# Performance work log

Hardware: AMD Instinct MI355X
Metric: run time of the kernel (lower is better)

Reference implementation:

```python
import jax, jax.numpy as jnp
import numpy as np

B = 2_000_000   # batch of affine transforms
N = 3           # spatial ndims -> flattened transform has N*(N+1)=12 entries


def setup_inputs() -> dict:
    key = jax.random.key(0)
    # small shifts so that identity + shift is always invertible
    trf = jax.random.normal(key, (B, N * (N + 1)), dtype=jnp.float32) * 0.1
    return {"trf": trf}


def reference(trf):
    """Batched equivalent of tf.map_fn(_single_invert, trf).

    Per sample: lift flattened (N,N+1) shift to an (N+1,N+1) matrix over the
    identity, invert it, and convert back to a flattened shift.
    """
    b = trf.shape[0]
    eye = jnp.eye(N + 1, dtype=trf.dtype)
    # affine_shift_to_identity: (b, N, N+1) -> pad zero row -> add identity
    mat = trf.reshape(b, N, N + 1)
    full = jnp.concatenate(
        [mat, jnp.zeros((b, 1, N + 1), dtype=trf.dtype)], axis=1
    ) + eye                                  # (b, N+1, N+1)
    inv = jnp.linalg.inv(full)               # batched tiny inversions
    # affine_identity_to_shift: subtract identity, drop last row, flatten
    shift = (inv - eye)[:, :N, :]            # (b, N, N+1)
    return shift.reshape(b, N * (N + 1))
```

## Files before the change

kernel.cpp:

```cpp
#include <hip/hip_runtime.h>


typedef float nfloat4 __attribute__((ext_vector_type(4)));

__global__ __launch_bounds__(256, 8) void invert_affine_kernel(
    const float4* __restrict__ in, float4* __restrict__ out, int b) {
  __shared__ float4 buf[768];

  const int tid = threadIdx.x;
  const int base_s = blockIdx.x * 256;
  const int base_f4 = base_s * 3;
  const int n_f4 = b * 3;

#pragma unroll
  for (int k = 0; k < 3; ++k) {
    int idx = base_f4 + k * 256 + tid;
    if (idx < n_f4) {
      nfloat4 nv = __builtin_nontemporal_load((const nfloat4*)&in[idx]);
      buf[k * 256 + tid] = make_float4(nv.x, nv.y, nv.z, nv.w);
    }
  }
  __syncthreads();

  const int s = base_s + tid;
  if (s < b) {
    float4 r0 = buf[tid * 3 + 0];
    float4 r1 = buf[tid * 3 + 1];
    float4 r2 = buf[tid * 3 + 2];

    float a00 = r0.x + 1.0f, a01 = r0.y,        a02 = r0.z,        t0 = r0.w;
    float a10 = r1.x,        a11 = r1.y + 1.0f, a12 = r1.z,        t1 = r1.w;
    float a20 = r2.x,        a21 = r2.y,        a22 = r2.z + 1.0f, t2 = r2.w;

    float b00 = a11 * a22 - a12 * a21;
    float b01 = a02 * a21 - a01 * a22;
    float b02 = a01 * a12 - a02 * a11;
    float b10 = a12 * a20 - a10 * a22;
    float b11 = a00 * a22 - a02 * a20;
    float b12 = a02 * a10 - a00 * a12;
    float b20 = a10 * a21 - a11 * a20;
    float b21 = a01 * a20 - a00 * a21;
    float b22 = a00 * a11 - a01 * a10;

    float det = a00 * b00 + a01 * b10 + a02 * b20;
    float rdet = 1.0f / det;

    b00 *= rdet; b01 *= rdet; b02 *= rdet;
    b10 *= rdet; b11 *= rdet; b12 *= rdet;
    b20 *= rdet; b21 *= rdet; b22 *= rdet;

    buf[tid * 3 + 0] = make_float4(b00 - 1.0f, b01, b02,
                                   -(b00 * t0 + b01 * t1 + b02 * t2));
    buf[tid * 3 + 1] = make_float4(b10, b11 - 1.0f, b12,
                                   -(b10 * t0 + b11 * t1 + b12 * t2));
    buf[tid * 3 + 2] = make_float4(b20, b21, b22 - 1.0f,
                                   -(b20 * t0 + b21 * t1 + b22 * t2));
  }
  __syncthreads();

#pragma unroll
  for (int k = 0; k < 3; ++k) {
    int idx = base_f4 + k * 256 + tid;
    if (idx < n_f4) {
      float4 vv = buf[k * 256 + tid];
      nfloat4 nv;
      nv.x = vv.x; nv.y = vv.y; nv.z = vv.z; nv.w = vv.w;
      __builtin_nontemporal_store(nv, (nfloat4*)&out[idx]);
    }
  }
}

extern "C" void kernel_launch(void* const* d_in, const int* in_sizes, int n_in,
                              void* d_out, int out_size, void* d_ws, size_t ws_size,
                              hipStream_t stream) {
  const float4* trf = (const float4*)d_in[0];
  float4* out = (float4*)d_out;
  int b = in_sizes[0] / 12;
  const int threads = 256;
  int blocks = (b + threads - 1) / threads;
  invert_affine_kernel<<<blocks, threads, 0, stream>>>(trf, out, b);
}
```

Before: 160.3 us.

## Use per-wave shared buffers with wave barriers and two samples per thread

Each block is split into four independent waves, and each wave stages 128 samples in its own slice of shared memory. This lets the block-wide __syncthreads be replaced by wave-level barriers. Every thread now processes two samples, so half as many blocks are launched, and the occupancy hint drops from 8 to 6. The aim is to remove block-level synchronisation stalls and per-block overhead in this memory-bound kernel. The cost is more shared memory per block, which may lower occupancy.

```diff
diff --git a/kernel.cpp b/kernel.cpp
--- a/kernel.cpp
+++ b/kernel.cpp
@@ -3,66 +3,73 @@
 
 typedef float nfloat4 __attribute__((ext_vector_type(4)));
 
-__global__ __launch_bounds__(256, 8) void invert_affine_kernel(
+__global__ __launch_bounds__(256, 6) void invert_affine_kernel(
     const float4* __restrict__ in, float4* __restrict__ out, int b) {
-  __shared__ float4 buf[768];
+  __shared__ float4 buf[4][384];
 
-  const int tid = threadIdx.x;
-  const int base_s = blockIdx.x * 256;
-  const int base_f4 = base_s * 3;
+  const int wave = threadIdx.x >> 6;
+  const int lane = threadIdx.x & 63;
+  float4* wbuf = buf[wave];
+
+  const int s0 = blockIdx.x * 512 + wave * 128;
+  const int base_f4 = s0 * 3;
   const int n_f4 = b * 3;
 
 #pragma unroll
-  for (int k = 0; k < 3; ++k) {
-    int idx = base_f4 + k * 256 + tid;
+  for (int k = 0; k < 6; ++k) {
+    const int idx = base_f4 + k * 64 + lane;
     if (idx < n_f4) {
       nfloat4 nv = __builtin_nontemporal_load((const nfloat4*)&in[idx]);
-      buf[k * 256 + tid] = make_float4(nv.x, nv.y, nv.z, nv.w);
+      wbuf[k * 64 + lane] = make_float4(nv.x, nv.y, nv.z, nv.w);
     }
   }
-  __syncthreads();
-
-  const int s = base_s + tid;
-  if (s < b) {
-    float4 r0 = buf[tid * 3 + 0];
-    float4 r1 = buf[tid * 3 + 1];
-    float4 r2 = buf[tid * 3 + 2];
-
-    float a00 = r0.x + 1.0f, a01 = r0.y,        a02 = r0.z,        t0 = r0.w;
-    float a10 = r1.x,        a11 = r1.y + 1.0f, a12 = r1.z,        t1 = r1.w;
-    float a20 = r2.x,        a21 = r2.y,        a22 = r2.z + 1.0f, t2 = r2.w;
-
-    float b00 = a11 * a22 - a12 * a21;
-    float b01 = a02 * a21 - a01 * a22;
-    float b02 = a01 * a12 - a02 * a11;
-    float b10 = a12 * a20 - a10 * a22;
-    float b11 = a00 * a22 - a02 * a20;
-    float b12 = a02 * a10 - a00 * a12;
-    float b20 = a10 * a21 - a11 * a20;
-    float b21 = a01 * a20 - a00 * a21;
-    float b22 = a00 * a11 - a01 * a10;
-
-    float det = a00 * b00 + a01 * b10 + a02 * b20;
-    float rdet = 1.0f / det;
-
-    b00 *= rdet; b01 *= rdet; b02 *= rdet;
-    b10 *= rdet; b11 *= rdet; b12 *= rdet;
-    b20 *= rdet; b21 *= rdet; b22 *= rdet;
-
-    buf[tid * 3 + 0] = make_float4(b00 - 1.0f, b01, b02,
-                                   -(b00 * t0 + b01 * t1 + b02 * t2));
-    buf[tid * 3 + 1] = make_float4(b10, b11 - 1.0f, b12,
-                                   -(b10 * t0 + b11 * t1 + b12 * t2));
-    buf[tid * 3 + 2] = make_float4(b20, b21, b22 - 1.0f,
-                                   -(b20 * t0 + b21 * t1 + b22 * t2));
-  }
-  __syncthreads();
+  __builtin_amdgcn_wave_barrier();
 
 #pragma unroll
-  for (int k = 0; k < 3; ++k) {
-    int idx = base_f4 + k * 256 + tid;
+  for (int si = 0; si < 2; ++si) {
+    const int s = s0 + si * 64 + lane;
+    if (s < b) {
+      const int o = (si * 64 + lane) * 3;
+      float4 r0 = wbuf[o + 0];
+      float4 r1 = wbuf[o + 1];
+      float4 r2 = wbuf[o + 2];
+
+      float a00 = r0.x + 1.0f, a01 = r0.y,        a02 = r0.z,        t0 = r0.w;
+      float a10 = r1.x,        a11 = r1.y + 1.0f, a12 = r1.z,        t1 = r1.w;
+      float a20 = r2.x,        a21 = r2.y,        a22 = r2.z + 1.0f, t2 = r2.w;
+
+      float b00 = a11 * a22 - a12 * a21;
+      float b01 = a02 * a21 - a01 * a22;
+      float b02 = a01 * a12 - a02 * a11;
+      float b10 = a12 * a20 - a10 * a22;
+      float b11 = a00 * a22 - a02 * a20;
+      float b12 = a02 * a10 - a00 * a12;
+      float b20 = a10 * a21 - a11 * a20;
+      float b21 = a01 * a20 - a00 * a21;
+      float b22 = a00 * a11 - a01 * a10;
+
+      float det = a00 * b00 + a01 * b10 + a02 * b20;
+      float rdet = 1.0f / det;
+
+      b00 *= rdet; b01 *= rdet; b02 *= rdet;
+      b10 *= rdet; b11 *= rdet; b12 *= rdet;
+      b20 *= rdet; b21 *= rdet; b22 *= rdet;
+
+      wbuf[o + 0] = make_float4(b00 - 1.0f, b01, b02,
+                                -(b00 * t0 + b01 * t1 + b02 * t2));
+      wbuf[o + 1] = make_float4(b10, b11 - 1.0f, b12,
+                                -(b10 * t0 + b11 * t1 + b12 * t2));
+      wbuf[o + 2] = make_float4(b20, b21, b22 - 1.0f,
+                                -(b20 * t0 + b21 * t1 + b22 * t2));
+    }
+  }
+  __builtin_amdgcn_wave_barrier();
+
+#pragma unroll
+  for (int k = 0; k < 6; ++k) {
+    const int idx = base_f4 + k * 64 + lane;
     if (idx < n_f4) {
-      float4 vv = buf[k * 256 + tid];
+      const float4 vv = wbuf[k * 64 + lane];
       nfloat4 nv;
       nv.x = vv.x; nv.y = vv.y; nv.z = vv.z; nv.w = vv.w;
       __builtin_nontemporal_store(nv, (nfloat4*)&out[idx]);
@@ -77,6 +84,7 @@
   float4* out = (float4*)d_out;
   int b = in_sizes[0] / 12;
   const int threads = 256;
-  int blocks = (b + threads - 1) / threads;
+  const int samples_per_block = 512;
+  int blocks = (b + samples_per_block - 1) / samples_per_block;
   invert_affine_kernel<<<blocks, threads, 0, stream>>>(trf, out, b);
 }
```

New measurement: 159.7 us. About the same (-0.4%).
